# Kernel tuning notes

Hardware: AMD Instinct MI355X
Metric: run time of the kernel (lower is better)

The kernel has to match this reference:

```python
import jax, jax.numpy as jnp
import numpy as np
import math

B, S, DM = 2, 2048, 2048
NH, NKV, HD = 16, 4, 128
DFF = 8192
K_KEEP = DFF // 2  # sparsity_ratio = 0.5
EPS = 1e-6


def setup_inputs() -> dict:
    key = jax.random.key(0)
    ks = jax.random.split(key, 10)
    sc = 0.02
    return {
        "hidden_states": jax.random.normal(ks[0], (B, S, DM), dtype=jnp.float32),
        "wq": jax.random.normal(ks[1], (NH * HD, DM), dtype=jnp.float32) * sc,
        "wk": jax.random.normal(ks[2], (NKV * HD, DM), dtype=jnp.float32) * sc,
        "wv": jax.random.normal(ks[3], (NKV * HD, DM), dtype=jnp.float32) * sc,
        "wo": jax.random.normal(ks[4], (DM, NH * HD), dtype=jnp.float32) * sc,
        "ln1_w": jnp.ones((DM,), dtype=jnp.float32),
        "ln2_w": jnp.ones((DM,), dtype=jnp.float32),
        "w_gate": jax.random.normal(ks[5], (DFF, DM), dtype=jnp.float32) * sc,
        "w_up": jax.random.normal(ks[6], (DFF, DM), dtype=jnp.float32) * sc,
        "w_down": jax.random.normal(ks[7], (DM, DFF), dtype=jnp.float32) * sc,
    }


def _rmsnorm(x, w):
    var = jnp.mean(x * x, axis=-1, keepdims=True)
    return x * jax.lax.rsqrt(var + EPS) * w


def reference(hidden_states, wq, wk, wv, wo, ln1_w, ln2_w, w_gate, w_up, w_down):
    b, s, _ = hidden_states.shape
    # --- attention sub-block: RMSNorm -> GQA causal attention -> residual ---
    x = _rmsnorm(hidden_states, ln1_w)
    q = (x @ wq.T).reshape(b, s, NH, HD)
    k = (x @ wk.T).reshape(b, s, NKV, HD)
    v = (x @ wv.T).reshape(b, s, NKV, HD)
    # expand KV heads to match query heads (GQA)
    rep = NH // NKV
    k = jnp.repeat(k, rep, axis=2)
    v = jnp.repeat(v, rep, axis=2)
    scores = jnp.einsum('bqhd,bkhd->bhqk', q, k) / math.sqrt(HD)
    causal = jnp.tril(jnp.ones((s, s), dtype=bool))
    scores = jnp.where(causal, scores, jnp.finfo(scores.dtype).min)
    attn = jax.nn.softmax(scores, axis=-1)
    o = jnp.einsum('bhqk,bkhd->bqhd', attn, v).reshape(b, s, NH * HD)
    h = hidden_states + o @ wo.T
    # --- FFN sub-block: RMSNorm -> TopK-sparse SwiGLU -> residual ---
    y = _rmsnorm(h, ln2_w)
    gate = jax.nn.silu(y @ w_gate.T)  # [b, s, DFF]
    mag = jnp.abs(gate)
    thr = jax.lax.top_k(mag, K_KEEP)[0][..., -1:]  # kth-largest magnitude
    gate = jnp.where(mag >= thr, gate, 0.0)
    ff = (gate * (y @ w_up.T)) @ w_down.T
    return h + ff
```

## Files before the change

kernel.cpp:

```cpp
#include <hip/hip_runtime.h>
#include <stdint.h>

constexpr int SEQ    = 2048;
constexpr int DMODEL = 2048;
constexpr int NHEADS = 16;
constexpr int NKVH   = 4;
constexpr int HDIM   = 128;
constexpr int DFFN   = 8192;
constexpr int BATCH  = 2;
constexpr int MTOK   = BATCH * SEQ;
constexpr int KKEEP  = DFFN / 2;

typedef __bf16 bf16x8 __attribute__((ext_vector_type(8)));
typedef float  f32x4  __attribute__((ext_vector_type(4)));
typedef float  f32x16 __attribute__((ext_vector_type(16)));
typedef unsigned short u16;
typedef unsigned int   u32;

__device__ __forceinline__ u16 f2bu(float f) {
  u32 x = __builtin_bit_cast(u32, f);
  return (u16)((x + 0x7FFFu + ((x >> 16) & 1u)) >> 16);
}
__device__ __forceinline__ float b2f(u16 u) {
  u32 v = ((u32)u) << 16;
  return __builtin_bit_cast(float, v);
}
__device__ __forceinline__ void gl_lds16(const void* g, void* l) {
  __builtin_amdgcn_global_load_lds((const __attribute__((address_space(1))) u32*)g,
                                   (__attribute__((address_space(3))) u32*)l, 16, 0, 0);
}

__global__ __launch_bounds__(256) void cvt_kernel(const float* __restrict__ in,
                                                  u16* __restrict__ out, int n) {
  int i = (blockIdx.x * 256 + threadIdx.x) * 4;
  if (i >= n) return;
  float4 v = *(const float4*)(in + i);
  uint2 pk;
  pk.x = (u32)f2bu(v.x) | ((u32)f2bu(v.y) << 16);
  pk.y = (u32)f2bu(v.z) | ((u32)f2bu(v.w) << 16);
  *(uint2*)(out + i) = pk;
}

__global__ __launch_bounds__(256) void rmsnorm_kernel(const float* __restrict__ in,
                                                      const float* __restrict__ w,
                                                      u16* __restrict__ out) {
  const int tid = threadIdx.x;
  const size_t row = blockIdx.x;
  const float* x = in + row * DMODEL;
  float4 v0 = *(const float4*)(x + tid * 4);
  float4 v1 = *(const float4*)(x + 1024 + tid * 4);
  float s = v0.x*v0.x + v0.y*v0.y + v0.z*v0.z + v0.w*v0.w
          + v1.x*v1.x + v1.y*v1.y + v1.z*v1.z + v1.w*v1.w;
#pragma unroll
  for (int off = 1; off < 64; off <<= 1) s += __shfl_xor(s, off, 64);
  __shared__ float wsum[4];
  if ((tid & 63) == 0) wsum[tid >> 6] = s;
  __syncthreads();
  s = wsum[0] + wsum[1] + wsum[2] + wsum[3];
  const float rinv = rsqrtf(s * (1.0f / DMODEL) + 1e-6f);
  u16* o = out + row * DMODEL;
#pragma unroll
  for (int part = 0; part < 2; ++part) {
    int c = part * 1024 + tid * 4;
    float4 vv = (part == 0) ? v0 : v1;
    float4 wv = *(const float4*)(w + c);
    uint2 pk;
    pk.x = (u32)f2bu(vv.x * rinv * wv.x) | ((u32)f2bu(vv.y * rinv * wv.y) << 16);
    pk.y = (u32)f2bu(vv.z * rinv * wv.z) | ((u32)f2bu(vv.w * rinv * wv.w) << 16);
    *(uint2*)(o + c) = pk;
  }
}

template <int EPI>
__global__ __launch_bounds__(256, 2)
void gemm_bt(const u16* __restrict__ A, const u16* __restrict__ B,
             void* __restrict__ C, const float* res,
             int M, int N, int K) {
  __shared__ u16 As[2][128 * 64];
  __shared__ u16 Bs[2][128 * 64];
  const int tid = threadIdx.x;
  const int wave = tid >> 6, lane = tid & 63;
  const int nwg = gridDim.x * gridDim.y;
  const int lin = blockIdx.y * gridDim.x + blockIdx.x;
  const int swz = (lin & 7) * (nwg >> 3) + (lin >> 3);
  const int m0 = (swz / gridDim.x) * 128, n0 = (swz % gridDim.x) * 128;
  const int r_in = lane >> 3, chk = lane & 7;
  const int fk = lane >> 4, fc = lane & 15;
  const int wm = (wave >> 1) * 64, wn = (wave & 1) * 64;
  const int nt = K >> 6;
  f32x4 acc[4][4] = {};

  auto stage = [&](int buf, int t) {
    const int kt = t * 64;
#pragma unroll
    for (int i = 0; i < 4; ++i) {
      int row = wave * 32 + i * 8 + r_in;
      int gc = chk ^ (row & 7);
      gl_lds16(A + (size_t)(m0 + row) * K + kt + gc * 8, &As[buf][(wave * 32 + i * 8) * 64]);
    }
#pragma unroll
    for (int i = 0; i < 4; ++i) {
      int row = wave * 32 + i * 8 + r_in;
      int gc = chk ^ (row & 7);
      gl_lds16(B + (size_t)(n0 + row) * K + kt + gc * 8, &Bs[buf][(wave * 32 + i * 8) * 64]);
    }
  };

  stage(0, 0);
  asm volatile("s_waitcnt vmcnt(0)" ::: "memory");
  __builtin_amdgcn_s_barrier();

  for (int t = 0; t < nt; ++t) {
    if (t + 1 < nt) stage((t + 1) & 1, t + 1);
    const u16* Ab = As[t & 1];
    const u16* Bb = Bs[t & 1];
#pragma unroll
    for (int kk = 0; kk < 2; ++kk) {
      bf16x8 a[4], b[4];
#pragma unroll
      for (int i = 0; i < 4; ++i) {
        int row = wm + i * 16 + fc;
        int c = (kk * 4 + fk) ^ (row & 7);
        a[i] = *(const bf16x8*)(Ab + row * 64 + c * 8);
      }
#pragma unroll
      for (int j = 0; j < 4; ++j) {
        int row = wn + j * 16 + fc;
        int c = (kk * 4 + fk) ^ (row & 7);
        b[j] = *(const bf16x8*)(Bb + row * 64 + c * 8);
      }
#pragma unroll
      for (int i = 0; i < 4; ++i)
#pragma unroll
        for (int j = 0; j < 4; ++j)
          acc[i][j] = __builtin_amdgcn_mfma_f32_16x16x32_bf16(a[i], b[j], acc[i][j], 0, 0, 0);
    }
    asm volatile("s_waitcnt vmcnt(0)" ::: "memory");
    __builtin_amdgcn_s_barrier();
  }

  const int rb = fk * 4;
#pragma unroll
  for (int i = 0; i < 4; ++i) {
#pragma unroll
    for (int j = 0; j < 4; ++j) {
      int row = m0 + wm + i * 16 + rb;
      int col = n0 + wn + j * 16 + fc;
      f32x4 v = acc[i][j];
      if constexpr (EPI == 0) {
        u16* o = (u16*)C;
#pragma unroll
        for (int r = 0; r < 4; ++r) o[(size_t)(row + r) * N + col] = f2bu(v[r]);
      } else if constexpr (EPI == 1) {
        u16* o = (u16*)C;
        int bb = row >> 11, s = row & (SEQ - 1);
        int kvh = col >> 7, d = col & (HDIM - 1);
        size_t base = (((size_t)bb * NKVH + kvh) * HDIM + d) * SEQ + s;
        uint2 pk;
        pk.x = (u32)f2bu(v[0]) | ((u32)f2bu(v[1]) << 16);
        pk.y = (u32)f2bu(v[2]) | ((u32)f2bu(v[3]) << 16);
        *(uint2*)(o + base) = pk;
      } else if constexpr (EPI == 2) {
        float* o = (float*)C;
#pragma unroll
        for (int r = 0; r < 4; ++r) {
          size_t idx = (size_t)(row + r) * N + col;
          float rv = res[idx];
          o[idx] = v[r] + rv;
        }
      } else {
        float* o = (float*)C;
#pragma unroll
        for (int r = 0; r < 4; ++r) {
          float g = v[r];
          o[(size_t)(row + r) * N + col] = g / (1.0f + __expf(-g));
        }
      }
    }
  }
}

template <int EPI>
__global__ __launch_bounds__(512, 2)
void gemm256(const u16* __restrict__ A, const u16* __restrict__ B,
             void* __restrict__ C, int M, int N, int K) {
  __shared__ u16 As[2][2][128 * 32];
  __shared__ u16 Bs[2][2][128 * 32];
  const int tid = threadIdx.x;
  const int wave = tid >> 6, lane = tid & 63;
  const int nwg = gridDim.x * gridDim.y;
  const int lin = blockIdx.y * gridDim.x + blockIdx.x;
  const int swz = (lin & 7) * (nwg >> 3) + (lin >> 3);
  const int m0 = (swz / gridDim.x) * 256, n0 = (swz % gridDim.x) * 256;
  const int wm = wave >> 2, wn = wave & 3;
  const int fk = lane >> 4, fc = lane & 15;
  const int nt = K >> 5;
  const int s_row = (wave * 64 + lane) >> 2;
  const int s_gc = (lane & 3) ^ ((s_row >> 1) & 3);
  f32x4 acc[8][4] = {};

  auto stageA = [&](int buf, int t) {
    const int kt = t * 32;
#pragma unroll
    for (int h = 0; h < 2; ++h)
      gl_lds16(A + (size_t)(m0 + h * 128 + s_row) * K + kt + s_gc * 8,
               &As[buf][h][wave * 512]);
  };
  auto stageB = [&](int buf, int t) {
    const int kt = t * 32;
#pragma unroll
    for (int h = 0; h < 2; ++h)
      gl_lds16(B + (size_t)(n0 + h * 128 + s_row) * K + kt + s_gc * 8,
               &Bs[buf][h][wave * 512]);
  };

  stageA(0, 0); stageB(0, 0);
  asm volatile("s_waitcnt vmcnt(0)" ::: "memory");
  __builtin_amdgcn_s_barrier();

  for (int t = 0; t < nt; ++t) {
    const int buf = t & 1, nxt = buf ^ 1;
    const u16* Ab = &As[buf][wm][0];
    const u16* Bb = &Bs[buf][wn >> 1][0];
    bf16x8 a[4], b[4];
    if (t + 1 < nt) stageA(nxt, t + 1);
#pragma unroll
    for (int n = 0; n < 4; ++n) {
      int row = (wn & 1) * 64 + n * 16 + fc;
      int slot = fk ^ ((row >> 1) & 3);
      b[n] = *(const bf16x8*)(Bb + row * 32 + slot * 8);
    }
#pragma unroll
    for (int m = 0; m < 4; ++m) {
      int row = m * 16 + fc;
      int slot = fk ^ ((row >> 1) & 3);
      a[m] = *(const bf16x8*)(Ab + row * 32 + slot * 8);
    }
    __builtin_amdgcn_s_barrier();
    asm volatile("s_waitcnt lgkmcnt(0)" ::: "memory");
    __builtin_amdgcn_sched_barrier(0);
    __builtin_amdgcn_s_setprio(1);
#pragma unroll
    for (int m = 0; m < 4; ++m)
#pragma unroll
      for (int n = 0; n < 4; ++n)
        acc[m][n] = __builtin_amdgcn_mfma_f32_16x16x32_bf16(a[m], b[n], acc[m][n], 0, 0, 0);
    __builtin_amdgcn_s_setprio(0);
    __builtin_amdgcn_s_barrier();
    if (t + 1 < nt) stageB(nxt, t + 1);
#pragma unroll
    for (int m = 0; m < 4; ++m) {
      int row = (m + 4) * 16 + fc;
      int slot = fk ^ ((row >> 1) & 3);
      a[m] = *(const bf16x8*)(Ab + row * 32 + slot * 8);
    }
    __builtin_amdgcn_s_barrier();
    asm volatile("s_waitcnt lgkmcnt(0)" ::: "memory");
    __builtin_amdgcn_sched_barrier(0);
    __builtin_amdgcn_s_setprio(1);
#pragma unroll
    for (int m = 0; m < 4; ++m)
#pragma unroll
      for (int n = 0; n < 4; ++n)
        acc[m + 4][n] = __builtin_amdgcn_mfma_f32_16x16x32_bf16(a[m], b[n], acc[m + 4][n], 0, 0, 0);
    __builtin_amdgcn_s_setprio(0);
    if (t + 1 < nt) asm volatile("s_waitcnt vmcnt(0)" ::: "memory");
    __builtin_amdgcn_s_barrier();
  }

  const int rb = fk * 4;
#pragma unroll
  for (int m = 0; m < 8; ++m) {
#pragma unroll
    for (int n = 0; n < 4; ++n) {
      int row = m0 + wm * 128 + m * 16 + rb;
      int col = n0 + wn * 64 + n * 16 + fc;
      f32x4 v = acc[m][n];
      if constexpr (EPI == 0) {
        u16* o = (u16*)C;
#pragma unroll
        for (int r = 0; r < 4; ++r) o[(size_t)(row + r) * N + col] = f2bu(v[r]);
      } else {
        float* o = (float*)C;
#pragma unroll
        for (int r = 0; r < 4; ++r) {
          float g = v[r];
          o[(size_t)(row + r) * N + col] = g / (1.0f + __expf(-g));
        }
      }
    }
  }
}

__global__ __launch_bounds__(256, 2)
void attn_kernel(const u16* __restrict__ Q, const u16* __restrict__ Kb,
                 const u16* __restrict__ Vt, u16* __restrict__ O) {
  __shared__ u16 Ksh[2 * 32 * 128];
  __shared__ u16 Vsh[2 * 128 * 32];
  const int tid = threadIdx.x, wave = tid >> 6, lane = tid & 63;
  const int half = lane >> 5, l31 = lane & 31;
  const int d_lin = blockIdx.x + gridDim.x * (blockIdx.y + gridDim.y * blockIdx.z);
  const int lin = (d_lin & 7) * 64 + (d_lin >> 3);
  const int bx = lin & 15, h = (lin >> 4) & 15, b = lin >> 8;
  const int kvh = h >> 2;
  const int qw = bx * 128 + wave * 32;
  const float SC = 0.08838834764831845f;
  const int ntb = bx * 4 + 4;
  const int nmy = bx * 4 + wave;

  bf16x8 qf[8];
  {
    const u16* qp = Q + ((size_t)(b * SEQ + qw + l31)) * DMODEL + h * HDIM + half * 8;
#pragma unroll
    for (int s = 0; s < 8; ++s) qf[s] = *(const bf16x8*)(qp + s * 16);
  }
  f32x16 oacc[4] = {};
  float m_run = -1e30f, l_run = 0.0f;
  const size_t vbase = ((size_t)(b * NKVH + kvh)) * HDIM * SEQ;
  const u16* kbase = Kb + (size_t)b * SEQ * (NKVH * HDIM) + kvh * HDIM;

  auto stage = [&](int bi, int k0) {
    u16* Kd = Ksh + bi * 4096;
    u16* Vd = Vsh + bi * 4096;
#pragma unroll
    for (int ii = 0; ii < 2; ++ii) {
      int inst = wave * 2 + ii;
      {
        int row = inst * 4 + (lane >> 4);
        int c = (lane & 15) ^ (row & 15);
        gl_lds16(kbase + (size_t)(k0 + row) * (NKVH * HDIM) + c * 8, Kd + inst * 512);
      }
      {
        int row = inst * 16 + (lane >> 2);
        int c = (lane & 3) ^ ((row >> 1) & 3);
        gl_lds16(Vt + vbase + (size_t)row * SEQ + k0 + c * 8, Vd + inst * 512);
      }
    }
  };

  stage(0, 0);
  __syncthreads();

  for (int t = 0; t < ntb; ++t) {
    if (t + 1 < ntb) stage((t + 1) & 1, (t + 1) * 32);
    if (t <= nmy) {
      const u16* Kd = Ksh + (t & 1) * 4096;
      const u16* Vd = Vsh + (t & 1) * 4096;
      f32x16 st = {};
#pragma unroll
      for (int s = 0; s < 8; ++s) {
        int c = (half + 2 * s) ^ (l31 & 15);
        bf16x8 kf = *(const bf16x8*)(Kd + l31 * 128 + c * 8);
        st = __builtin_amdgcn_mfma_f32_32x32x16_bf16(kf, qf[s], st, 0, 0, 0);
      }
      const bool diag = (t * 32 == qw);
      float sv[16];
#pragma unroll
      for (int r = 0; r < 16; ++r) {
        float x = st[r] * SC;
        if (diag) {
          int kvl = (r & 3) + 8 * (r >> 2) + 4 * half;
          if (kvl > l31) x = -1e30f;
        }
        sv[r] = x;
      }
      float mx = sv[0];
#pragma unroll
      for (int r = 1; r < 16; ++r) mx = fmaxf(mx, sv[r]);
      mx = fmaxf(mx, __shfl_xor(mx, 32, 64));
      if (__any(mx > m_run + 4.0f)) {
        float mnew = fmaxf(m_run, mx);
        float alpha = __expf(m_run - mnew);
        m_run = mnew;
        l_run *= alpha;
#pragma unroll
        for (int r = 0; r < 16; ++r) {
          float ar = __shfl(alpha, (r & 3) + 8 * (r >> 2) + 4 * half, 64);
#pragma unroll
          for (int dt = 0; dt < 4; ++dt) oacc[dt][r] *= ar;
        }
      }
      float p[16];
      float rs = 0.0f;
#pragma unroll
      for (int r = 0; r < 16; ++r) { p[r] = __expf(sv[r] - m_run); rs += p[r]; }
      rs += __shfl_xor(rs, 32, 64);
      l_run += rs;
      u32 c01 = (u32)f2bu(p[0])  | ((u32)f2bu(p[1])  << 16);
      u32 c23 = (u32)f2bu(p[2])  | ((u32)f2bu(p[3])  << 16);
      u32 c45 = (u32)f2bu(p[4])  | ((u32)f2bu(p[5])  << 16);
      u32 c67 = (u32)f2bu(p[6])  | ((u32)f2bu(p[7])  << 16);
      u32 c89 = (u32)f2bu(p[8])  | ((u32)f2bu(p[9])  << 16);
      u32 cAB = (u32)f2bu(p[10]) | ((u32)f2bu(p[11]) << 16);
      u32 cCD = (u32)f2bu(p[12]) | ((u32)f2bu(p[13]) << 16);
      u32 cEF = (u32)f2bu(p[14]) | ((u32)f2bu(p[15]) << 16);
      u32 paw[2][4];
      {
        u32 sA = __shfl_xor(c01, 32, 64), sB = __shfl_xor(c23, 32, 64);
        u32 sC = __shfl_xor(c45, 32, 64), sD = __shfl_xor(c67, 32, 64);
        paw[0][0] = half ? sC : c01;  paw[0][1] = half ? sD : c23;
        paw[0][2] = half ? c45 : sA;  paw[0][3] = half ? c67 : sB;
      }
      {
        u32 sA = __shfl_xor(c89, 32, 64), sB = __shfl_xor(cAB, 32, 64);
        u32 sC = __shfl_xor(cCD, 32, 64), sD = __shfl_xor(cEF, 32, 64);
        paw[1][0] = half ? sC : c89;  paw[1][1] = half ? sD : cAB;
        paw[1][2] = half ? cCD : sA;  paw[1][3] = half ? cEF : sB;
      }
#pragma unroll
      for (int ks = 0; ks < 2; ++ks) {
        bf16x8 paf = __builtin_bit_cast(bf16x8, *(uint4*)&paw[ks][0]);
#pragma unroll
        for (int dt = 0; dt < 4; ++dt) {
          int row = dt * 32 + l31;
          int c = (half + 2 * ks) ^ ((row >> 1) & 3);
          bf16x8 vf = *(const bf16x8*)(Vd + row * 32 + c * 8);
          oacc[dt] = __builtin_amdgcn_mfma_f32_32x32x16_bf16(paf, vf, oacc[dt], 0, 0, 0);
        }
      }
    }
    __syncthreads();
  }

  float rinv = 1.0f / l_run;
  u16* ob = O + ((size_t)(b * SEQ + qw)) * DMODEL + h * HDIM + l31;
#pragma unroll
  for (int r = 0; r < 16; ++r) {
    int qr = (r & 3) + 8 * (r >> 2) + 4 * half;
    float ir = __shfl(rinv, qr, 64);
#pragma unroll
    for (int dt = 0; dt < 4; ++dt)
      ob[(size_t)qr * DMODEL + dt * 32] = f2bu(oacc[dt][r] * ir);
  }
}

__global__ __launch_bounds__(256)
void topk_kernel(const float* __restrict__ gate, u16* __restrict__ upact) {
  __shared__ u32 sabs[DFFN];
  __shared__ u32 hist[4][256];
  __shared__ u32 ss[257];
  __shared__ u32 sh_prefix, sh_rem;
  const int tid = threadIdx.x, wave = tid >> 6;
  const size_t row = blockIdx.x;
  const float* g = gate + row * DFFN;
  for (int it = 0; it < 4; ++it) {
    int e = it * 2048 + tid * 8;
    float4 a = *(const float4*)(g + e);
    float4 b = *(const float4*)(g + e + 4);
    sabs[e + 0] = __builtin_bit_cast(u32, a.x);
    sabs[e + 1] = __builtin_bit_cast(u32, a.y);
    sabs[e + 2] = __builtin_bit_cast(u32, a.z);
    sabs[e + 3] = __builtin_bit_cast(u32, a.w);
    sabs[e + 4] = __builtin_bit_cast(u32, b.x);
    sabs[e + 5] = __builtin_bit_cast(u32, b.y);
    sabs[e + 6] = __builtin_bit_cast(u32, b.z);
    sabs[e + 7] = __builtin_bit_cast(u32, b.w);
  }
  if (tid == 0) { sh_prefix = 0; sh_rem = KKEEP; }
  __syncthreads();
  for (int pass = 0; pass < 4; ++pass) {
    const int p = 24 - pass * 8;
    const u32 mask_hi = (pass == 0) ? 0u : (0xFFFFFFFFu << (p + 8));
    for (int i = tid; i < 1024; i += 256) ((u32*)hist)[i] = 0;
    __syncthreads();
    const u32 prefix = sh_prefix, rem = sh_rem;
    for (int it = 0; it < 4; ++it) {
      int e = it * 2048 + tid * 8;
#pragma unroll
      for (int j = 0; j < 8; ++j) {
        u32 mg = sabs[e + j] & 0x7FFFFFFFu;
        if ((mg & mask_hi) == (prefix & mask_hi))
          atomicAdd(&hist[wave][(mg >> p) & 0xFF], 1u);
      }
    }
    __syncthreads();
    ss[tid] = hist[0][tid] + hist[1][tid] + hist[2][tid] + hist[3][tid];
    if (tid == 0) ss[256] = 0;
    __syncthreads();
    for (int off = 1; off < 256; off <<= 1) {
      u32 v = (tid + off < 256) ? ss[tid + off] : 0u;
      __syncthreads();
      ss[tid] += v;
      __syncthreads();
    }
    if (ss[tid] >= rem && ss[tid + 1] < rem) {
      sh_prefix = prefix | ((u32)tid << p);
      sh_rem = rem - ss[tid + 1];
    }
    __syncthreads();
  }
  const u32 thr = sh_prefix;
  u16* ua = upact + row * DFFN;
  for (int it = 0; it < 4; ++it) {
    int e = it * 2048 + tid * 8;
    uint4 uv = *(const uint4*)(ua + e);
    const u16* up16 = (const u16*)&uv;
    u16 outp[8];
#pragma unroll
    for (int j = 0; j < 8; ++j) {
      u32 bits = sabs[e + j];
      u32 mg = bits & 0x7FFFFFFFu;
      float gg = __builtin_bit_cast(float, bits);
      float prod = (mg >= thr) ? gg * b2f(up16[j]) : 0.0f;
      outp[j] = f2bu(prod);
    }
    uint4 ov;
    ov.x = (u32)outp[0] | ((u32)outp[1] << 16);
    ov.y = (u32)outp[2] | ((u32)outp[3] << 16);
    ov.z = (u32)outp[4] | ((u32)outp[5] << 16);
    ov.w = (u32)outp[6] | ((u32)outp[7] << 16);
    *(uint4*)(ua + e) = ov;
  }
}

extern "C" void kernel_launch(void* const* d_in, const int* in_sizes, int n_in,
                              void* d_out, int out_size, void* d_ws, size_t ws_size,
                              hipStream_t stream) {
  const float* hidden = (const float*)d_in[0];
  const float* wq = (const float*)d_in[1];
  const float* wk = (const float*)d_in[2];
  const float* wv = (const float*)d_in[3];
  const float* wo = (const float*)d_in[4];
  const float* ln1 = (const float*)d_in[5];
  const float* ln2 = (const float*)d_in[6];
  const float* wg = (const float*)d_in[7];
  const float* wu = (const float*)d_in[8];
  const float* wd = (const float*)d_in[9];
  float* out = (float*)d_out;
  (void)in_sizes; (void)n_in; (void)out_size;

  size_t off = 0;
  auto alloc = [&](size_t n) { char* r = (char*)d_ws + off; off += (n + 255) & ~(size_t)255; return r; };
  u16* wq_b = (u16*)alloc((size_t)DMODEL * DMODEL * 2);
  u16* wk_b = (u16*)alloc((size_t)NKVH * HDIM * DMODEL * 2);
  u16* wv_b = (u16*)alloc((size_t)NKVH * HDIM * DMODEL * 2);
  u16* wo_b = (u16*)alloc((size_t)DMODEL * DMODEL * 2);
  u16* wg_b = (u16*)alloc((size_t)DFFN * DMODEL * 2);
  u16* tok  = (u16*)alloc((size_t)MTOK * DMODEL * 2);
  u16* upb  = (u16*)alloc((size_t)MTOK * DFFN * 2);
  char* S   = alloc((size_t)(MTOK / 2) * DFFN * 4);
  u16* qb   = (u16*)S;
  u16* kb   = (u16*)(S + (size_t)MTOK * DMODEL * 2);
  u16* vtb  = (u16*)(S + (size_t)MTOK * DMODEL * 2 + (size_t)MTOK * NKVH * HDIM * 2);
  u16* wu_b = (u16*)(S + (size_t)MTOK * DMODEL * 2 + 2 * (size_t)MTOK * NKVH * HDIM * 2);
  float* gateh = (float*)S;
  u16* wd_b = (u16*)S;
  const size_t needed = off;
  if (ws_size < needed) return;

  auto cvt = [&](const float* src, u16* dst, size_t n) {
    cvt_kernel<<<dim3((unsigned)(n / 1024)), 256, 0, stream>>>(src, dst, (int)n);
  };
  cvt(wq, wq_b, (size_t)DMODEL * DMODEL);
  cvt(wk, wk_b, (size_t)NKVH * HDIM * DMODEL);
  cvt(wv, wv_b, (size_t)NKVH * HDIM * DMODEL);
  cvt(wo, wo_b, (size_t)DMODEL * DMODEL);
  cvt(wg, wg_b, (size_t)DFFN * DMODEL);
  cvt(wu, wu_b, (size_t)DFFN * DMODEL);

  rmsnorm_kernel<<<MTOK, 256, 0, stream>>>(hidden, ln1, tok);

  gemm_bt<0><<<dim3(DMODEL / 128, MTOK / 128), 256, 0, stream>>>(
      tok, wq_b, qb, nullptr, MTOK, DMODEL, DMODEL);
  gemm_bt<0><<<dim3(NKVH * HDIM / 128, MTOK / 128), 256, 0, stream>>>(
      tok, wk_b, kb, nullptr, MTOK, NKVH * HDIM, DMODEL);
  gemm_bt<1><<<dim3(NKVH * HDIM / 128, MTOK / 128), 256, 0, stream>>>(
      tok, wv_b, vtb, nullptr, MTOK, NKVH * HDIM, DMODEL);

  attn_kernel<<<dim3(SEQ / 128, NHEADS, BATCH), 256, 0, stream>>>(qb, kb, vtb, tok);

  gemm_bt<2><<<dim3(DMODEL / 128, MTOK / 128), 256, 0, stream>>>(
      tok, wo_b, out, hidden, MTOK, DMODEL, DMODEL);

  rmsnorm_kernel<<<MTOK, 256, 0, stream>>>(out, ln2, tok);

  gemm256<0><<<dim3(DFFN / 256, MTOK / 256), 512, 0, stream>>>(
      tok, wu_b, upb, MTOK, DFFN, DMODEL);

  for (int half = 0; half < 2; ++half) {
    const u16* yh = tok + (size_t)half * (MTOK / 2) * DMODEL;
    u16* uph = upb + (size_t)half * (MTOK / 2) * DFFN;
    gemm256<3><<<dim3(DFFN / 256, (MTOK / 2) / 256), 512, 0, stream>>>(
        yh, wg_b, gateh, MTOK / 2, DFFN, DMODEL);
    topk_kernel<<<MTOK / 2, 256, 0, stream>>>(gateh, uph);
  }

  cvt(wd, wd_b, (size_t)DMODEL * DFFN);

  gemm_bt<2><<<dim3(DMODEL / 128, MTOK / 128), 256, 0, stream>>>(
      upb, wd_b, out, out, MTOK, DMODEL, DFFN);
}
```

Before: 1.104 ms.

## Deepen GEMM K-tile to 64 with interleaved staging; reorder attention block schedule

The 256x256 GEMM now stages 64-wide K tiles with an 8-slot XOR swizzle. Loads for the next tiles are spread across four MFMA sub-phases, with partial vmcnt waits so more global traffic stays in flight per barrier. This aims to cut barrier and latency overhead per K step, at the cost of doubling LDS use, which may limit occupancy. Separately, the attention block-to-work mapping now pairs each causal query block with its mirror (q and 15-q) across the two grid halves to balance causal work across CUs.

```diff
diff --git a/kernel.cpp b/kernel.cpp
--- a/kernel.cpp
+++ b/kernel.cpp
@@ -184,8 +184,8 @@
 __global__ __launch_bounds__(512, 2)
 void gemm256(const u16* __restrict__ A, const u16* __restrict__ B,
              void* __restrict__ C, int M, int N, int K) {
-  __shared__ u16 As[2][2][128 * 32];
-  __shared__ u16 Bs[2][2][128 * 32];
+  __shared__ u16 As[2][2][128 * 64];
+  __shared__ u16 Bs[2][2][128 * 64];
   const int tid = threadIdx.x;
   const int wave = tid >> 6, lane = tid & 63;
   const int nwg = gridDim.x * gridDim.y;
@@ -194,97 +194,121 @@
   const int m0 = (swz / gridDim.x) * 256, n0 = (swz % gridDim.x) * 256;
   const int wm = wave >> 2, wn = wave & 3;
   const int fk = lane >> 4, fc = lane & 15;
-  const int nt = K >> 5;
-  const int s_row = (wave * 64 + lane) >> 2;
-  const int s_gc = (lane & 3) ^ ((s_row >> 1) & 3);
+  const int nt = K >> 6, ni = nt >> 1;
+  const int s_sub = lane >> 3;
+  const int s_gc  = (lane & 7) ^ s_sub;
   f32x4 acc[8][4] = {};
-
-  auto stageA = [&](int buf, int t) {
-    const int kt = t * 32;
-#pragma unroll
-    for (int h = 0; h < 2; ++h)
-      gl_lds16(A + (size_t)(m0 + h * 128 + s_row) * K + kt + s_gc * 8,
-               &As[buf][h][wave * 512]);
-  };
-  auto stageB = [&](int buf, int t) {
-    const int kt = t * 32;
-#pragma unroll
-    for (int h = 0; h < 2; ++h)
-      gl_lds16(B + (size_t)(n0 + h * 128 + s_row) * K + kt + s_gc * 8,
-               &Bs[buf][h][wave * 512]);
-  };
-
-  stageA(0, 0); stageB(0, 0);
-  asm volatile("s_waitcnt vmcnt(0)" ::: "memory");
-  __builtin_amdgcn_s_barrier();
-
-  for (int t = 0; t < nt; ++t) {
-    const int buf = t & 1, nxt = buf ^ 1;
-    const u16* Ab = &As[buf][wm][0];
-    const u16* Bb = &Bs[buf][wn >> 1][0];
-    bf16x8 a[4], b[4];
-    if (t + 1 < nt) stageA(nxt, t + 1);
+  bf16x8 b0[4], b1[4], a[4];
+
+  auto sA = [&](int buf, int h, int t) {
+    const u16* src = A + (size_t)(m0 + h * 128) * K + t * 64;
+    u16* dst = &As[buf][h][0];
+#pragma unroll
+    for (int I = 0; I < 2; ++I) {
+      int row = I * 64 + wave * 8 + s_sub;
+      gl_lds16(src + (size_t)row * K + s_gc * 8, dst + (I * 512 + wave * 64) * 8);
+    }
+  };
+  auto sB = [&](int buf, int h, int t) {
+    const u16* src = B + (size_t)(n0 + h * 128) * K + t * 64;
+    u16* dst = &Bs[buf][h][0];
+#pragma unroll
+    for (int I = 0; I < 2; ++I) {
+      int row = I * 64 + wave * 8 + s_sub;
+      gl_lds16(src + (size_t)row * K + s_gc * 8, dst + (I * 512 + wave * 64) * 8);
+    }
+  };
+  auto rb = [&](const u16* Bh) {
 #pragma unroll
     for (int n = 0; n < 4; ++n) {
       int row = (wn & 1) * 64 + n * 16 + fc;
-      int slot = fk ^ ((row >> 1) & 3);
-      b[n] = *(const bf16x8*)(Bb + row * 32 + slot * 8);
-    }
+      b0[n] = *(const bf16x8*)(Bh + row * 64 + ((fk) ^ (row & 7)) * 8);
+      b1[n] = *(const bf16x8*)(Bh + row * 64 + ((4 + fk) ^ (row & 7)) * 8);
+    }
+  };
+  auto ra = [&](const u16* Ah, int mh, int kk) {
 #pragma unroll
     for (int m = 0; m < 4; ++m) {
-      int row = m * 16 + fc;
-      int slot = fk ^ ((row >> 1) & 3);
-      a[m] = *(const bf16x8*)(Ab + row * 32 + slot * 8);
-    }
+      int row = mh * 64 + m * 16 + fc;
+      a[m] = *(const bf16x8*)(Ah + row * 64 + ((kk * 4 + fk) ^ (row & 7)) * 8);
+    }
+  };
+  auto midbar = [&]() {
     __builtin_amdgcn_s_barrier();
     asm volatile("s_waitcnt lgkmcnt(0)" ::: "memory");
     __builtin_amdgcn_sched_barrier(0);
     __builtin_amdgcn_s_setprio(1);
-#pragma unroll
-    for (int m = 0; m < 4; ++m)
-#pragma unroll
-      for (int n = 0; n < 4; ++n)
-        acc[m][n] = __builtin_amdgcn_mfma_f32_16x16x32_bf16(a[m], b[n], acc[m][n], 0, 0, 0);
+  };
+  auto endbar = [&]() {
     __builtin_amdgcn_s_setprio(0);
     __builtin_amdgcn_s_barrier();
-    if (t + 1 < nt) stageB(nxt, t + 1);
-#pragma unroll
-    for (int m = 0; m < 4; ++m) {
-      int row = (m + 4) * 16 + fc;
-      int slot = fk ^ ((row >> 1) & 3);
-      a[m] = *(const bf16x8*)(Ab + row * 32 + slot * 8);
-    }
+  };
+  auto mfma16 = [&](int mh, bf16x8* bb) {
+#pragma unroll
+    for (int m = 0; m < 4; ++m)
+#pragma unroll
+      for (int n = 0; n < 4; ++n)
+        acc[mh * 4 + m][n] =
+            __builtin_amdgcn_mfma_f32_16x16x32_bf16(a[m], bb[n], acc[mh * 4 + m][n], 0, 0, 0);
+  };
+
+  sB(0, 0, 0); sB(0, 1, 0);
+  sA(0, 0, 0); sA(0, 1, 0);
+  sB(1, 0, 1); sB(1, 1, 1);
+  asm volatile("s_waitcnt vmcnt(4)" ::: "memory");
+  __builtin_amdgcn_s_barrier();
+
+  for (int i = 0; i < ni; ++i) {
+    const int u = 2 * i, v = 2 * i + 1;
+    const bool more = (i + 1 < ni);
+    const u16* Au = &As[0][wm][0];
+    const u16* Bu = &Bs[0][wn >> 1][0];
+    const u16* Av = &As[1][wm][0];
+    const u16* Bv = &Bs[1][wn >> 1][0];
+    rb(Bu); ra(Au, 0, 0); sA(1, 0, v);
+    midbar(); mfma16(0, b0); endbar();
+    ra(Au, 1, 0); sA(1, 1, v);
+    midbar(); mfma16(1, b0); endbar();
+    ra(Au, 0, 1); if (more) sB(0, 0, u + 2);
+    midbar(); mfma16(0, b1); endbar();
+    ra(Au, 1, 1); if (more) sB(0, 1, u + 2);
+    midbar(); mfma16(1, b1);
+    __builtin_amdgcn_s_setprio(0);
+    if (more) asm volatile("s_waitcnt vmcnt(4)" ::: "memory");
+    else      asm volatile("s_waitcnt vmcnt(0)" ::: "memory");
     __builtin_amdgcn_s_barrier();
-    asm volatile("s_waitcnt lgkmcnt(0)" ::: "memory");
-    __builtin_amdgcn_sched_barrier(0);
-    __builtin_amdgcn_s_setprio(1);
-#pragma unroll
-    for (int m = 0; m < 4; ++m)
-#pragma unroll
-      for (int n = 0; n < 4; ++n)
-        acc[m + 4][n] = __builtin_amdgcn_mfma_f32_16x16x32_bf16(a[m], b[n], acc[m + 4][n], 0, 0, 0);
+    rb(Bv); ra(Av, 0, 0); if (more) sA(0, 0, u + 2);
+    midbar(); mfma16(0, b0); endbar();
+    ra(Av, 1, 0); if (more) sA(0, 1, u + 2);
+    midbar(); mfma16(1, b0); endbar();
+    ra(Av, 0, 1); if (more) sB(1, 0, v + 2);
+    midbar(); mfma16(0, b1); endbar();
+    ra(Av, 1, 1); if (more) sB(1, 1, v + 2);
+    midbar(); mfma16(1, b1);
     __builtin_amdgcn_s_setprio(0);
-    if (t + 1 < nt) asm volatile("s_waitcnt vmcnt(0)" ::: "memory");
+    if (more) {
+      asm volatile("s_waitcnt vmcnt(4)" ::: "memory");
+    }
     __builtin_amdgcn_s_barrier();
   }
 
-  const int rb = fk * 4;
+  const int rbase = fk * 4;
 #pragma unroll
   for (int m = 0; m < 8; ++m) {
 #pragma unroll
     for (int n = 0; n < 4; ++n) {
-      int row = m0 + wm * 128 + m * 16 + rb;
+      int row = m0 + wm * 128 + m * 16 + rbase;
       int col = n0 + wn * 64 + n * 16 + fc;
-      f32x4 v = acc[m][n];
+      f32x4 vv = acc[m][n];
       if constexpr (EPI == 0) {
         u16* o = (u16*)C;
 #pragma unroll
-        for (int r = 0; r < 4; ++r) o[(size_t)(row + r) * N + col] = f2bu(v[r]);
+        for (int r = 0; r < 4; ++r) o[(size_t)(row + r) * N + col] = f2bu(vv[r]);
       } else {
         float* o = (float*)C;
 #pragma unroll
         for (int r = 0; r < 4; ++r) {
-          float g = v[r];
+          float g = vv[r];
           o[(size_t)(row + r) * N + col] = g / (1.0f + __expf(-g));
         }
       }
@@ -300,8 +324,10 @@
   const int tid = threadIdx.x, wave = tid >> 6, lane = tid & 63;
   const int half = lane >> 5, l31 = lane & 31;
   const int d_lin = blockIdx.x + gridDim.x * (blockIdx.y + gridDim.y * blockIdx.z);
-  const int lin = (d_lin & 7) * 64 + (d_lin >> 3);
-  const int bx = lin & 15, h = (lin >> 4) & 15, b = lin >> 8;
+  const int x = d_lin & 255, hi = d_lin >> 8;
+  const int e = (x & 7) * 32 + (x >> 3);
+  const int q = e & 7, h = (e >> 3) & 15, b = e >> 7;
+  const int bx = hi ? 15 - q : q;
   const int kvh = h >> 2;
   const int qw = bx * 128 + wave * 32;
   const float SC = 0.08838834764831845f;
@@ -357,12 +383,12 @@
       float sv[16];
 #pragma unroll
       for (int r = 0; r < 16; ++r) {
-        float x = st[r] * SC;
+        float xx = st[r] * SC;
         if (diag) {
           int kvl = (r & 3) + 8 * (r >> 2) + 4 * half;
-          if (kvl > l31) x = -1e30f;
+          if (kvl > l31) xx = -1e30f;
         }
-        sv[r] = x;
+        sv[r] = xx;
       }
       float mx = sv[0];
 #pragma unroll
```

Result: faster. 986.2 us (-10.7%).
